# Performance work log

Measured on AMD Instinct MI355X. Metric: run time of the kernel, lower is better.

## Reference

```python
import jax, jax.numpy as jnp
import numpy as np
from jax import lax

# SparseLSTM(input_size=1024, hidden_size=1024, blocks=4, density=0.5)
# input segments: width 512 at starts [0,170,341,512] (overlapping)
# output segments: contiguous quarters of 256
K = 4
IB = 512   # per-block input width
HB = 256   # per-block hidden width
STARTS = (0, 170, 341, 512)


def setup_inputs() -> dict:
    key = jax.random.key(0)
    ks = jax.random.split(key, 8)
    T, B, D = 512, 64, 1024
    std = 1.0 / np.sqrt(HB)
    return {
        "x":  jax.random.normal(ks[0], (T, B, D), jnp.float32),
        "h0": jax.random.normal(ks[1], (1, B, D), jnp.float32),
        "c0": jax.random.normal(ks[2], (1, B, D), jnp.float32),
        # stacked per-block LSTM params, PyTorch gate order (i, f, g, o)
        "W_ih": jax.random.uniform(ks[3], (K, 4 * HB, IB), jnp.float32, -std, std),
        "W_hh": jax.random.uniform(ks[4], (K, 4 * HB, HB), jnp.float32, -std, std),
        "b_ih": jax.random.uniform(ks[5], (K, 4 * HB), jnp.float32, -std, std),
        "b_hh": jax.random.uniform(ks[6], (K, 4 * HB), jnp.float32, -std, std),
    }


def _sparse_lstm(x, h0, c0, W_ih, W_hh, b_ih, b_hh):
    T, B, _ = x.shape
    # gather overlapping input slices -> [k, T, B, IB]
    xb = jnp.stack([lax.slice_in_dim(x, s, s + IB, axis=2) for s in STARTS])
    # contiguous hidden quarters -> [k, B, HB]
    hb = h0[0].reshape(B, K, HB).transpose(1, 0, 2)
    cb = c0[0].reshape(B, K, HB).transpose(1, 0, 2)
    # precompute input contributions to gates: [T, k, B, 4*HB]
    xg = jnp.einsum("ktbi,kgi->tkbg", xb, W_ih) + (b_ih + b_hh)[None, :, None, :]

    def step(carry, xg_t):
        h, c = carry  # each [k, B, HB]
        gates = xg_t + jnp.einsum("kbh,kgh->kbg", h, W_hh)
        i, f, g, o = jnp.split(gates, 4, axis=-1)
        c = jax.nn.sigmoid(f) * c + jax.nn.sigmoid(i) * jnp.tanh(g)
        h = jax.nn.sigmoid(o) * jnp.tanh(c)
        return (h, c), h

    (hT, cT), ys = lax.scan(step, (hb, cb), xg)  # ys: [T, k, B, HB]
    output = ys.transpose(0, 2, 1, 3).reshape(T, B, K * HB)
    new_h = hT.transpose(1, 0, 2).reshape(B, K * HB)[None]
    new_c = cT.transpose(1, 0, 2).reshape(B, K * HB)[None]
    return output, new_h, new_c


def reference(x, h0, c0, W_ih, W_hh, b_ih, b_hh):
    return _sparse_lstm(x, h0, c0, W_ih, W_hh, b_ih, b_hh)
```

## Files before the change

kernel.cpp:

```cpp
#include <hip/hip_runtime.h>

typedef _Float16 half8   __attribute__((ext_vector_type(8)));
typedef _Float16 half2_t __attribute__((ext_vector_type(2)));
typedef float    floatx4 __attribute__((ext_vector_type(4)));
typedef unsigned int uintx4 __attribute__((ext_vector_type(4)));
typedef unsigned int uint32;

__device__ __forceinline__ float sigm(float v) { return 1.0f / (1.0f + __expf(-v)); }
__device__ __forceinline__ float tanh_(float v) { float e = __expf(2.0f * v); return (e - 1.0f) / (e + 1.0f); }

__device__ __forceinline__ int dot4(uint32 a, uint32 b, int c) {
#if __has_builtin(__builtin_amdgcn_sdot4)
  return __builtin_amdgcn_sdot4((int)a, (int)b, c, false);
#else
  int r = c;
  r += (int)(char)(a)       * (int)(char)(b);
  r += (int)(char)(a >> 8)  * (int)(char)(b >> 8);
  r += (int)(char)(a >> 16) * (int)(char)(b >> 16);
  r += (int)(char)(a >> 24) * (int)(char)(b >> 24);
  return r;
#endif
}

__device__ __forceinline__ uint32 pack_rte(float a, float b) {
  half2_t h; h[0] = (_Float16)a; h[1] = (_Float16)b;
  return __builtin_bit_cast(uint32, h);
}

__global__ __launch_bounds__(256) void pack_wih(const float* __restrict__ wih, uint32* __restrict__ wihd) {
  int p = blockIdx.x * 256 + threadIdx.x;
  wihd[p] = pack_rte(wih[2 * p], wih[2 * p + 1]);
}

__global__ __launch_bounds__(256) void pack_whh8(const float* __restrict__ whh, uintx4* __restrict__ wq8) {
  int p = blockIdx.x * 256 + threadIdx.x;
  int row = p & 1023, qi = (p >> 10) & 3, qt = (p >> 12) & 3, kk = p >> 14;
  const float* src = whh + ((size_t)(kk * 1024 + row)) * 256 + qt * 64 + qi * 16;
  uint32 dw[4];
#pragma unroll
  for (int d = 0; d < 4; ++d) {
    uint32 v = 0;
#pragma unroll
    for (int e = 0; e < 4; ++e) {
      int q = (int)rintf(src[d * 4 + e] * 2032.0f);
      q = q > 127 ? 127 : (q < -127 ? -127 : q);
      v |= ((uint32)(q & 0xff)) << (8 * e);
    }
    dw[d] = v;
  }
  wq8[p] = (uintx4){dw[0], dw[1], dw[2], dw[3]};
}

__global__ __launch_bounds__(256) void pack_x_all(const float* __restrict__ x, uint32* __restrict__ xsd) {
  for (long p = (long)blockIdx.x * 256 + threadIdx.x; p < 33554432L; p += 2097152L) {
    int chunk = (int)(p >> 21);
    int r = (int)(p & 2097151);
    int k  = r >> 19;
    int R  = (r >> 8) & 2047;
    int pc = r & 255;
    int b = R >> 5, ct = R & 31;
    int t = chunk * 32 + ct;
    int sk = (k * 1024) / 6;
    const float* src = x + ((size_t)t * 64 + b) * 1024 + sk + pc * 2;
    xsd[p] = pack_rte(src[0], src[1]);
  }
}

__global__ __launch_bounds__(256) void gemm_all(const _Float16* __restrict__ xs,
                                                const _Float16* __restrict__ wih16,
                                                const float* __restrict__ bih,
                                                const float* __restrict__ bhh,
                                                _Float16* __restrict__ xg) {
  __shared__ _Float16 SL[18432];
  const int tid = threadIdx.x;
  const int bid = blockIdx.x;
  const int chunk = bid >> 9;
  const int b9 = bid & 511;
  const int nt = b9 & 7, mt = (b9 >> 3) & 15, kb = b9 >> 7;
  const int l = tid & 63;
  const int wid = tid >> 6;
  const int wm = wid >> 1, wn = wid & 1;
  const int lr = l & 15, lk = l >> 4;

  floatx4 acc[4][4] = {};
  const _Float16* xsk = xs + ((size_t)(chunk * 4 + kb) << 20);
  const _Float16* wk  = wih16 + ((size_t)kb << 19);

  for (int kt = 0; kt < 8; ++kt) {
    const int K0 = kt * 64;
    half8 av[4], bv[4];
#pragma unroll
    for (int q = 0; q < 4; ++q) {
      int s = q * 256 + tid;
      int row = s >> 3, c8 = s & 7;
      av[q] = *(const half8*)(xsk + (size_t)(mt * 128 + row) * 512 + K0 + c8 * 8);
      bv[q] = *(const half8*)(wk  + (size_t)(nt * 128 + row) * 512 + K0 + c8 * 8);
    }
#pragma unroll
    for (int q = 0; q < 4; ++q) {
      int s = q * 256 + tid;
      int row = s >> 3, c8 = s & 7;
      *(half8*)&SL[row * 72 + c8 * 8]        = av[q];
      *(half8*)&SL[9216 + row * 72 + c8 * 8] = bv[q];
    }
    __syncthreads();
#pragma unroll
    for (int ks = 0; ks < 2; ++ks) {
      half8 af[4], bf[4];
#pragma unroll
      for (int fm = 0; fm < 4; ++fm)
        af[fm] = *(const half8*)&SL[(wm * 64 + fm * 16 + lr) * 72 + (ks * 4 + lk) * 8];
#pragma unroll
      for (int fn = 0; fn < 4; ++fn)
        bf[fn] = *(const half8*)&SL[9216 + (wn * 64 + fn * 16 + lr) * 72 + (ks * 4 + lk) * 8];
#pragma unroll
      for (int fm = 0; fm < 4; ++fm)
#pragma unroll
        for (int fn = 0; fn < 4; ++fn)
          acc[fm][fn] = __builtin_amdgcn_mfma_f32_16x16x32_f16(af[fm], bf[fn], acc[fm][fn], 0, 0, 0);
    }
    __syncthreads();
  }
  float bias[4];
#pragma unroll
  for (int fn = 0; fn < 4; ++fn) {
    int g = nt * 128 + wn * 64 + fn * 16 + lr;
    bias[fn] = bih[kb * 1024 + g] + bhh[kb * 1024 + g];
  }
#pragma unroll
  for (int fm = 0; fm < 4; ++fm)
#pragma unroll
    for (int fn = 0; fn < 4; ++fn) {
      int colb = wn * 64 + fn * 16 + lr;
#pragma unroll
      for (int r = 0; r < 4; ++r) {
        int rowb = wm * 64 + fm * 16 + lk * 4 + r;
        SL[rowb * 128 + colb] = (_Float16)(acc[fm][fn][r] + bias[fn]);
      }
    }
  __syncthreads();
#pragma unroll
  for (int q = 0; q < 8; ++q) {
    int s = q * 256 + tid;
    int row = s >> 4, c16 = s & 15;
    int R = mt * 128 + row;
    size_t off = ((size_t)(kb * 64 + (R >> 5)) * 512 + chunk * 32 + (R & 31)) * 1024 + nt * 128 + c16 * 8;
    *(uintx4*)(xg + off) = *(const uintx4*)&SL[row * 128 + c16 * 8];
  }
}

__global__ __launch_bounds__(512, 2)
void lstm_all(const _Float16* __restrict__ xg,
              const uintx4* __restrict__ wq8,
              const float* __restrict__ h0,
              const float* __restrict__ c0,
              float* __restrict__ out) {
  extern __shared__ uint32 lds[];
  unsigned char* h8   = (unsigned char*)lds;
  const _Float16* slab = (const _Float16*)(lds + 128);
  _Float16*      hist = (_Float16*)(lds + 4224);
  uintx4*        wl4  = (uintx4*)(lds + 5248);
  const int tid = threadIdx.x;
  const int j = tid >> 1, s = tid & 1;
  const int k = blockIdx.x >> 6, b = blockIdx.x & 63;

  const uintx4* wk = wq8 + ((size_t)k << 14);
#define LQ(g, i) uintx4 S##g##_##i = wk[(2 * s + ((i) >> 2)) * 4096 + ((i) & 3) * 1024 + (g) * 256 + j];
  LQ(0,0) LQ(0,1) LQ(0,2) LQ(0,3) LQ(0,4) LQ(0,5) LQ(0,6) LQ(0,7)
  LQ(1,0) LQ(1,1) LQ(1,2) LQ(1,3) LQ(1,4) LQ(1,5) LQ(1,6) LQ(1,7)
#undef LQ
#pragma unroll
  for (int i = 0; i < 8; ++i) {
    wl4[i * 512 + tid]       = wk[(2 * s + (i >> 2)) * 4096 + (i & 3) * 1024 + 512 + j];
    wl4[(8 + i) * 512 + tid] = wk[(2 * s + (i >> 2)) * 4096 + (i & 3) * 1024 + 768 + j];
  }

  const int gi = b * 1024 + k * 256 + j;
  float cst = c0[gi];
  float hn_prev = h0[gi];
  if (!s) {
    int q = (int)rintf(hn_prev * (127.0f / 8.0f));
    q = q > 127 ? 127 : (q < -127 ? -127 : q);
    h8[j] = (unsigned char)(q & 0xff);
  }

  const float DS1 = 0.0625f / 16129.0f;
  const float DS8 = 8.0f * DS1;

  const _Float16* xgp = xg + ((size_t)(k * 64 + b) << 19);

#define MQ(W, H, d) { d = dot4(W[0], H[0], d); d = dot4(W[1], H[1], d); \
                      d = dot4(W[2], H[2], d); d = dot4(W[3], H[3], d); }
#define STEPI(i) { uintx4 hq = hp4[s * 8 + (i)]; \
    MQ(S0_##i, hq, d0) MQ(S1_##i, hq, d1) \
    { uintx4 w = wl4[(i) * 512 + tid];       MQ(w, hq, d2) } \
    { uintx4 w = wl4[(8 + (i)) * 512 + tid]; MQ(w, hq, d3) } }

#pragma unroll 1
  for (int t = 0; t < 512; ++t) {
    if ((t & 7) == 0) {
      if (t) {
        int tb = t - 8;
#pragma unroll
        for (int q = 0; q < 4; ++q) {
          int idx = q * 512 + tid;
          int ct = idx >> 8, jj = idx & 255;
          out[((size_t)(tb + ct) * 64 + b) * 1024 + k * 256 + jj] = (float)hist[idx];
        }
      }
#pragma unroll
      for (int q = 0; q < 2; ++q)
        __builtin_amdgcn_global_load_lds(
            (const __attribute__((address_space(1))) void*)(xgp + (size_t)t * 1024 + q * 4096 + tid * 8),
            (__attribute__((address_space(3))) void*)(lds + 128 + q * 2048 + tid * 4), 16, 0, 0);
      asm volatile("s_waitcnt vmcnt(0)" ::: "memory");
      __syncthreads();
    }

    const uintx4* hp4 = (const uintx4*)(h8 + (t & 1) * 256);
    int d0 = 0, d1 = 0, d2 = 0, d3 = 0;
    STEPI(0) STEPI(1) STEPI(2) STEPI(3) STEPI(4) STEPI(5) STEPI(6) STEPI(7)

    d0 += __shfl_xor(d0, 1, 64);
    d1 += __shfl_xor(d1, 1, 64);
    d2 += __shfl_xor(d2, 1, 64);
    d3 += __shfl_xor(d3, 1, 64);

    const int ts = (t & 7) * 1024;
    float xi = (float)slab[ts + j];
    float xf = (float)slab[ts + 256 + j];
    float xgv = (float)slab[ts + 512 + j];
    float xo = (float)slab[ts + 768 + j];

    float dsc = (t == 0) ? DS8 : DS1;
    float iv = (float)d0 * dsc + xi;
    float fv = (float)d1 * dsc + xf;
    float gv = (float)d2 * dsc + xgv;
    float ov = (float)d3 * dsc + xo;
    float cn = sigm(fv) * cst + sigm(iv) * tanh_(gv);
    float hn = sigm(ov) * tanh_(cn);
    cst = cn; hn_prev = hn;
    if (!s) {
      hist[(t & 7) * 256 + j] = (_Float16)hn;
      int q = (int)rintf(hn * 127.0f);
      h8[((t & 1) ^ 1) * 256 + j] = (unsigned char)(q & 0xff);
    }
    __syncthreads();
  }
#undef MQ
#undef STEPI

#pragma unroll
  for (int q = 0; q < 4; ++q) {
    int idx = q * 512 + tid;
    int ct = idx >> 8, jj = idx & 255;
    out[((size_t)(504 + ct) * 64 + b) * 1024 + k * 256 + jj] = (float)hist[idx];
  }
  if (!s) {
    out[33554432 + gi] = hn_prev;
    out[33554432 + 65536 + gi] = cst;
  }
}

extern "C" void kernel_launch(void* const* d_in, const int* in_sizes, int n_in,
                              void* d_out, int out_size, void* d_ws, size_t ws_size,
                              hipStream_t stream) {
  const float* x   = (const float*)d_in[0];
  const float* h0  = (const float*)d_in[1];
  const float* c0  = (const float*)d_in[2];
  const float* Wih = (const float*)d_in[3];
  const float* Whh = (const float*)d_in[4];
  const float* bih = (const float*)d_in[5];
  const float* bhh = (const float*)d_in[6];
  float* out = (float*)d_out;
  char* ws = (char*)d_ws;

  _Float16* xg16  = (_Float16*)ws;
  _Float16* xs    = (_Float16*)(ws + 268435456L);
  _Float16* wih16 = (_Float16*)(ws + 402653184L);
  uintx4*   wq8   = (uintx4*)(ws + 406847488L);

  hipFuncSetAttribute((const void*)lstm_all, hipFuncAttributeMaxDynamicSharedMemorySize, 152064);

  pack_wih<<<4096, 256, 0, stream>>>(Wih, (uint32*)wih16);
  pack_whh8<<<256, 256, 0, stream>>>(Whh, wq8);
  pack_x_all<<<8192, 256, 0, stream>>>(x, (uint32*)xs);
  gemm_all<<<8192, 256, 0, stream>>>(xs, wih16, bih, bhh, xg16);
  lstm_all<<<256, 512, 152064, stream>>>(xg16, wq8, h0, c0, out);
}
```

Measured before the change: 1.016 ms.

## Split recurrent dot product across four threads per hidden unit

The recurrent LSTM kernel now runs 1024 threads per block, with four threads per hidden unit instead of two. Each thread covers a quarter of the hidden vector, and the partial gate sums are combined with two xor-shuffles. This halves the serial int8 dot-product chain per thread and the register-resident weight count, which shortens the per-timestep critical path. The cost is extra shuffles and redundant activation math across all four lanes, plus a 1024-thread barrier every step.

Measured after the change: 1.199 ms. +18.0%, slower.

```diff
diff --git a/kernel.cpp b/kernel.cpp
--- a/kernel.cpp
+++ b/kernel.cpp
@@ -149,7 +149,7 @@
   }
 }
 
-__global__ __launch_bounds__(512, 2)
+__global__ __launch_bounds__(1024, 4)
 void lstm_all(const _Float16* __restrict__ xg,
               const uintx4* __restrict__ wq8,
               const float* __restrict__ h0,
@@ -161,24 +161,22 @@
   _Float16*      hist = (_Float16*)(lds + 4224);
   uintx4*        wl4  = (uintx4*)(lds + 5248);
   const int tid = threadIdx.x;
-  const int j = tid >> 1, s = tid & 1;
+  const int j = tid >> 2, qt = tid & 3;
   const int k = blockIdx.x >> 6, b = blockIdx.x & 63;
 
-  const uintx4* wk = wq8 + ((size_t)k << 14);
-#define LQ(g, i) uintx4 S##g##_##i = wk[(2 * s + ((i) >> 2)) * 4096 + ((i) & 3) * 1024 + (g) * 256 + j];
-  LQ(0,0) LQ(0,1) LQ(0,2) LQ(0,3) LQ(0,4) LQ(0,5) LQ(0,6) LQ(0,7)
-  LQ(1,0) LQ(1,1) LQ(1,2) LQ(1,3) LQ(1,4) LQ(1,5) LQ(1,6) LQ(1,7)
-#undef LQ
-#pragma unroll
-  for (int i = 0; i < 8; ++i) {
-    wl4[i * 512 + tid]       = wk[(2 * s + (i >> 2)) * 4096 + (i & 3) * 1024 + 512 + j];
-    wl4[(8 + i) * 512 + tid] = wk[(2 * s + (i >> 2)) * 4096 + (i & 3) * 1024 + 768 + j];
+  const uintx4* wb = wq8 + ((size_t)(k * 4 + qt) << 12);
+  uintx4 S0_0 = wb[j],        S0_1 = wb[1024 + j],        S0_2 = wb[2048 + j],        S0_3 = wb[3072 + j];
+  uintx4 S3_0 = wb[768 + j],  S3_1 = wb[1024 + 768 + j],  S3_2 = wb[2048 + 768 + j],  S3_3 = wb[3072 + 768 + j];
+#pragma unroll
+  for (int i = 0; i < 4; ++i) {
+    wl4[i * 1024 + tid]       = wb[i * 1024 + 256 + j];
+    wl4[(4 + i) * 1024 + tid] = wb[i * 1024 + 512 + j];
   }
 
   const int gi = b * 1024 + k * 256 + j;
   float cst = c0[gi];
   float hn_prev = h0[gi];
-  if (!s) {
+  if (qt == 0) {
     int q = (int)rintf(hn_prev * (127.0f / 8.0f));
     q = q > 127 ? 127 : (q < -127 ? -127 : q);
     h8[j] = (unsigned char)(q & 0xff);
@@ -191,10 +189,11 @@
 
 #define MQ(W, H, d) { d = dot4(W[0], H[0], d); d = dot4(W[1], H[1], d); \
                       d = dot4(W[2], H[2], d); d = dot4(W[3], H[3], d); }
-#define STEPI(i) { uintx4 hq = hp4[s * 8 + (i)]; \
-    MQ(S0_##i, hq, d0) MQ(S1_##i, hq, d1) \
-    { uintx4 w = wl4[(i) * 512 + tid];       MQ(w, hq, d2) } \
-    { uintx4 w = wl4[(8 + (i)) * 512 + tid]; MQ(w, hq, d3) } }
+#define STEPI(i) { uintx4 hq = hp4[qt * 4 + (i)]; \
+    MQ(S0_##i, hq, d0) \
+    { uintx4 w = wl4[(i) * 1024 + tid];       MQ(w, hq, d1) } \
+    { uintx4 w = wl4[(4 + (i)) * 1024 + tid]; MQ(w, hq, d2) } \
+    MQ(S3_##i, hq, d3) }
 
 #pragma unroll 1
   for (int t = 0; t < 512; ++t) {
@@ -202,45 +201,39 @@
       if (t) {
         int tb = t - 8;
 #pragma unroll
-        for (int q = 0; q < 4; ++q) {
-          int idx = q * 512 + tid;
+        for (int q = 0; q < 2; ++q) {
+          int idx = q * 1024 + tid;
           int ct = idx >> 8, jj = idx & 255;
           out[((size_t)(tb + ct) * 64 + b) * 1024 + k * 256 + jj] = (float)hist[idx];
         }
       }
-#pragma unroll
-      for (int q = 0; q < 2; ++q)
-        __builtin_amdgcn_global_load_lds(
-            (const __attribute__((address_space(1))) void*)(xgp + (size_t)t * 1024 + q * 4096 + tid * 8),
-            (__attribute__((address_space(3))) void*)(lds + 128 + q * 2048 + tid * 4), 16, 0, 0);
+      __builtin_amdgcn_global_load_lds(
+          (const __attribute__((address_space(1))) void*)(xgp + (size_t)t * 1024 + tid * 8),
+          (__attribute__((address_space(3))) void*)(lds + 128 + tid * 4), 16, 0, 0);
       asm volatile("s_waitcnt vmcnt(0)" ::: "memory");
       __syncthreads();
     }
 
     const uintx4* hp4 = (const uintx4*)(h8 + (t & 1) * 256);
     int d0 = 0, d1 = 0, d2 = 0, d3 = 0;
-    STEPI(0) STEPI(1) STEPI(2) STEPI(3) STEPI(4) STEPI(5) STEPI(6) STEPI(7)
-
-    d0 += __shfl_xor(d0, 1, 64);
-    d1 += __shfl_xor(d1, 1, 64);
-    d2 += __shfl_xor(d2, 1, 64);
-    d3 += __shfl_xor(d3, 1, 64);
-
-    const int ts = (t & 7) * 1024;
-    float xi = (float)slab[ts + j];
-    float xf = (float)slab[ts + 256 + j];
-    float xgv = (float)slab[ts + 512 + j];
-    float xo = (float)slab[ts + 768 + j];
+    STEPI(0) STEPI(1) STEPI(2) STEPI(3)
+
+    float xv = (float)slab[(t & 7) * 1024 + qt * 256 + j];
 
     float dsc = (t == 0) ? DS8 : DS1;
-    float iv = (float)d0 * dsc + xi;
-    float fv = (float)d1 * dsc + xf;
-    float gv = (float)d2 * dsc + xgv;
-    float ov = (float)d3 * dsc + xo;
-    float cn = sigm(fv) * cst + sigm(iv) * tanh_(gv);
-    float hn = sigm(ov) * tanh_(cn);
+    float s0 = (float)d0 * dsc + ((qt == 0) ? xv : 0.0f);
+    float s1 = (float)d1 * dsc + ((qt == 1) ? xv : 0.0f);
+    float s2 = (float)d2 * dsc + ((qt == 2) ? xv : 0.0f);
+    float s3 = (float)d3 * dsc + ((qt == 3) ? xv : 0.0f);
+    s0 += __shfl_xor(s0, 1, 64); s0 += __shfl_xor(s0, 2, 64);
+    s1 += __shfl_xor(s1, 1, 64); s1 += __shfl_xor(s1, 2, 64);
+    s2 += __shfl_xor(s2, 1, 64); s2 += __shfl_xor(s2, 2, 64);
+    s3 += __shfl_xor(s3, 1, 64); s3 += __shfl_xor(s3, 2, 64);
+
+    float cn = sigm(s1) * cst + sigm(s0) * tanh_(s2);
+    float hn = sigm(s3) * tanh_(cn);
     cst = cn; hn_prev = hn;
-    if (!s) {
+    if (qt == 0) {
       hist[(t & 7) * 256 + j] = (_Float16)hn;
       int q = (int)rintf(hn * 127.0f);
       h8[((t & 1) ^ 1) * 256 + j] = (unsigned char)(q & 0xff);
@@ -251,15 +244,13 @@
 #undef STEPI
 
 #pragma unroll
-  for (int q = 0; q < 4; ++q) {
-    int idx = q * 512 + tid;
+  for (int q = 0; q < 2; ++q) {
+    int idx = q * 1024 + tid;
     int ct = idx >> 8, jj = idx & 255;
     out[((size_t)(504 + ct) * 64 + b) * 1024 + k * 256 + jj] = (float)hist[idx];
   }
-  if (!s) {
-    out[33554432 + gi] = hn_prev;
-    out[33554432 + 65536 + gi] = cst;
-  }
+  if (qt == 0) out[33554432 + gi] = hn_prev;
+  if (qt == 1) out[33554432 + 65536 + gi] = cst;
 }
 
 extern "C" void kernel_launch(void* const* d_in, const int* in_sizes, int n_in,
@@ -286,5 +277,5 @@
   pack_whh8<<<256, 256, 0, stream>>>(Whh, wq8);
   pack_x_all<<<8192, 256, 0, stream>>>(x, (uint32*)xs);
   gemm_all<<<8192, 256, 0, stream>>>(xs, wih16, bih, bhh, xg16);
-  lstm_all<<<256, 512, 152064, stream>>>(xg16, wq8, h0, c0, out);
-}
+  lstm_all<<<256, 1024, 152064, stream>>>(xg16, wq8, h0, c0, out);
+}
```
